# Kernel optimization log

Hardware: AMD Instinct MI355X
Metric: run time of the kernel (lower is better)

Reference implementation:

```python
import jax, jax.numpy as jnp
import numpy as np

N_NODES = 100_000
N_EDGES = 1_600_000
IN_DIM = 128
HIDDEN = 128
OUT_DIM = 64
N_LAYERS = 8
ALPHA = 0.1  # GCN2Conv alpha; beta = 1.0 since theta/layer not given


def setup_inputs() -> dict:
    key = jax.random.key(0)
    ks = jax.random.split(key, 6)
    x = jax.random.normal(ks[0], (N_NODES, IN_DIM), dtype=jnp.float32)
    edge_index = jax.random.randint(ks[1], (2, N_EDGES), 0, N_NODES, dtype=jnp.int64)
    W_in = jax.random.normal(ks[2], (IN_DIM, HIDDEN), dtype=jnp.float32) / np.sqrt(IN_DIM)
    b_in = jnp.zeros((HIDDEN,), jnp.float32)
    conv_w = jax.random.normal(ks[3], (N_LAYERS, HIDDEN, HIDDEN), dtype=jnp.float32) / np.sqrt(HIDDEN)
    W_out = jax.random.normal(ks[4], (HIDDEN, OUT_DIM), dtype=jnp.float32) / np.sqrt(HIDDEN)
    b_out = jnp.zeros((OUT_DIM,), jnp.float32)
    return {"x": x, "edge_index": edge_index, "W_in": W_in, "b_in": b_in,
            "conv_w": conv_w, "W_out": W_out, "b_out": b_out}


def reference(x, edge_index, W_in, b_in, conv_w, W_out, b_out):
    N = x.shape[0]
    # gcn_norm with self-loops: A_hat = D^-1/2 (A + I) D^-1/2
    loops = jnp.arange(N, dtype=edge_index.dtype)
    ei = jnp.concatenate([edge_index, jnp.stack([loops, loops])], axis=1)
    row, col = ei[0], ei[1]  # source, target
    deg = jax.ops.segment_sum(jnp.ones(ei.shape[1], x.dtype), col, num_segments=N)
    dinv = jnp.where(deg > 0, jax.lax.rsqrt(deg), 0.0)
    norm = dinv[row] * dinv[col]  # [E+N]

    h = jax.nn.relu(x @ W_in + b_in)  # input projection
    x0 = h  # initial residual
    for l in range(conv_w.shape[0]):
        # sparse neighbor aggregation: out[i] = sum_{(j->i)} norm * h[j]
        agg = jax.ops.segment_sum(h[row] * norm[:, None], col, num_segments=N)
        support = (1.0 - ALPHA) * agg + ALPHA * x0  # initial residual mix
        h = jax.nn.relu(support @ conv_w[l])  # beta=1 -> out = support @ W
        # dropout: identity in eval mode
    return h @ W_out + b_out
```

## Files before the change

kernel.cpp:

```cpp
#include <hip/hip_runtime.h>
#include <hip/hip_fp16.h>
#include <cstdint>
#include <cstddef>


#define HID 128
#define BKSH 9
#define RMAX 256
#define SLICE_CAP 11264

using f16x8 = __attribute__((ext_vector_type(8))) _Float16;
using f16x4 = __attribute__((ext_vector_type(4))) _Float16;
using f32x4 = __attribute__((ext_vector_type(4))) float;


__global__ __launch_bounds__(512) void k_bhist(const int* __restrict__ col, int E,
                                               int* __restrict__ bcnt, int R) {
  __shared__ int lh[RMAX];
  int tid = threadIdx.x;
  if (tid < R) lh[tid] = 0;
  __syncthreads();
  int base = blockIdx.x * 4096;
#pragma unroll
  for (int i = 0; i < 8; ++i) {
    int e = base + i * 512 + tid;
    if (e < E) atomicAdd(&lh[col[e] >> BKSH], 1);
  }
  __syncthreads();
  if (tid < R && lh[tid]) atomicAdd(&bcnt[tid], lh[tid]);
}

__global__ __launch_bounds__(256) void k_scan196(const int* __restrict__ bcnt,
                                                 int* __restrict__ gb,
                                                 int* __restrict__ gfront, int R) {
  __shared__ int s[256];
  int t = threadIdx.x;
  int v = (t < R) ? bcnt[t] : 0;
  s[t] = v;
  __syncthreads();
  for (int off = 1; off < 256; off <<= 1) {
    int a = (t >= off) ? s[t - off] : 0;
    __syncthreads();
    s[t] += a;
    __syncthreads();
  }
  int excl = s[t] - v;
  if (t < R) {
    gb[t] = excl;
    gfront[t] = excl;
  }
  if (t == 255) gb[R] = s[255];
}

__global__ __launch_bounds__(512) void k_partA(const int* __restrict__ row,
                                               const int* __restrict__ col, int E,
                                               int* __restrict__ gfront,
                                               int* __restrict__ tmp, int R) {
  __shared__ int lh[RMAX], base[RMAX], fr[RMAX];
  int tid = threadIdx.x;
  if (tid < R) { lh[tid] = 0; fr[tid] = 0; }
  __syncthreads();
  int b0 = blockIdx.x * 4096;
  int r[8], c[8], bk[8];
  bool ok[8];
#pragma unroll
  for (int i = 0; i < 8; ++i) {
    int e = b0 + i * 512 + tid;
    ok[i] = e < E;
    if (ok[i]) {
      r[i] = row[e];
      c[i] = col[e];
      bk[i] = c[i] >> BKSH;
      atomicAdd(&lh[bk[i]], 1);
    }
  }
  __syncthreads();
  if (tid < R && lh[tid] > 0) base[tid] = atomicAdd(&gfront[tid], lh[tid]);
  __syncthreads();
#pragma unroll
  for (int i = 0; i < 8; ++i) {
    if (ok[i]) {
      int o = atomicAdd(&fr[bk[i]], 1);
      tmp[base[bk[i]] + o] = (r[i] << BKSH) | (c[i] & ((1 << BKSH) - 1));
    }
  }
}

__global__ __launch_bounds__(512) void k_partB(const int* __restrict__ tmp,
                                               const int* __restrict__ gb,
                                               int* __restrict__ csr_src,
                                               int* __restrict__ row_ptr,
                                               float* __restrict__ dinv, int N, int E,
                                               int R) {
  __shared__ int h2[512], pref[512];
  __shared__ int slice[SLICE_CAP];
  int tid = threadIdx.x;
  int b = blockIdx.x;
  int lo = gb[b], hi = gb[b + 1];
  int cnt = hi - lo;
  h2[tid] = 0;
  __syncthreads();
  for (int k = tid; k < cnt; k += 512) atomicAdd(&h2[tmp[lo + k] & 511], 1);
  __syncthreads();
  int v = h2[tid];
  pref[tid] = v;
  __syncthreads();
  for (int off = 1; off < 512; off <<= 1) {
    int a = (tid >= off) ? pref[tid - off] : 0;
    __syncthreads();
    pref[tid] += a;
    __syncthreads();
  }
  int excl = pref[tid] - v;
  int node = b * 512 + tid;
  if (node < N) {
    row_ptr[node] = lo + excl;
    dinv[node] = rsqrtf((float)v + 1.0f);
  }
  if (b == R - 1 && tid == 0) row_ptr[N] = E;
  __syncthreads();
  pref[tid] = excl;
  h2[tid] = 0;
  __syncthreads();
  for (int k = tid; k < cnt; k += 512) {
    int ent = tmp[lo + k];
    int nd = ent & 511;
    int o = pref[nd] + atomicAdd(&h2[nd], 1);
    if (o < SLICE_CAP) slice[o] = ent >> BKSH;
    else csr_src[lo + o] = ent >> BKSH;
  }
  __syncthreads();
  int lim = cnt < SLICE_CAP ? cnt : SLICE_CAP;
  for (int k = tid; k < lim; k += 512) csr_src[lo + k] = slice[k];
}

__global__ void k_wprep(const float* __restrict__ Wc, const float* __restrict__ W_in,
                        const float* __restrict__ W_out, _Float16* __restrict__ Wt,
                        int L) {
  int id = blockIdx.x * blockDim.x + threadIdx.x;
  int nl = L * 16384;
  if (id < nl) {
    int l = id >> 14, r = id & 16383;
    int k = r >> 7, n = r & 127;
    Wt[(size_t)l * 16384 + n * 128 + k] = (_Float16)Wc[(size_t)l * 16384 + k * 128 + n];
  } else if (id < nl + 16384) {
    int r = id - nl;
    int k = r >> 7, n = r & 127;
    Wt[(size_t)nl + n * 128 + k] = (_Float16)W_in[k * 128 + n];
  } else if (id < nl + 16384 + 8192) {
    int r = id - nl - 16384;
    int k = r >> 6, n = r & 63;
    Wt[(size_t)(nl + 16384) + n * 128 + k] = (_Float16)W_out[k * 64 + n];
  }
}


__global__ __launch_bounds__(256) void k_aggregate(
    const _Float16* __restrict__ g, const _Float16* __restrict__ x0h,
    const float* __restrict__ dinv, const int* __restrict__ row_ptr,
    const int* __restrict__ csr_src, _Float16* __restrict__ support, int N) {
  int node = blockIdx.x * 8 + (threadIdx.x >> 5);
  if (node >= N) return;
  int lane = threadIdx.x & 31;
  int d0 = lane * 4;
  int beg = row_ptr[node], end = row_ptr[node + 1];
  float di = dinv[node];

  f16x4 v0 = *(const f16x4*)(g + (size_t)node * HID + d0);
  f16x4 xv = *(const f16x4*)(x0h + (size_t)node * HID + d0);

  float a0 = (float)v0[0], a1 = (float)v0[1];
  float a2 = (float)v0[2], a3 = (float)v0[3];

  int j = beg;
  for (; j + 8 <= end; j += 8) {
    int s0 = csr_src[j],     s1 = csr_src[j + 1], s2 = csr_src[j + 2], s3 = csr_src[j + 3];
    int s4 = csr_src[j + 4], s5 = csr_src[j + 5], s6 = csr_src[j + 6], s7 = csr_src[j + 7];
    f16x4 r0 = *(const f16x4*)(g + (size_t)s0 * HID + d0);
    f16x4 r1 = *(const f16x4*)(g + (size_t)s1 * HID + d0);
    f16x4 r2 = *(const f16x4*)(g + (size_t)s2 * HID + d0);
    f16x4 r3 = *(const f16x4*)(g + (size_t)s3 * HID + d0);
    f16x4 r4 = *(const f16x4*)(g + (size_t)s4 * HID + d0);
    f16x4 r5 = *(const f16x4*)(g + (size_t)s5 * HID + d0);
    f16x4 r6 = *(const f16x4*)(g + (size_t)s6 * HID + d0);
    f16x4 r7 = *(const f16x4*)(g + (size_t)s7 * HID + d0);
    a0 += (float)r0[0] + (float)r1[0] + (float)r2[0] + (float)r3[0] +
          (float)r4[0] + (float)r5[0] + (float)r6[0] + (float)r7[0];
    a1 += (float)r0[1] + (float)r1[1] + (float)r2[1] + (float)r3[1] +
          (float)r4[1] + (float)r5[1] + (float)r6[1] + (float)r7[1];
    a2 += (float)r0[2] + (float)r1[2] + (float)r2[2] + (float)r3[2] +
          (float)r4[2] + (float)r5[2] + (float)r6[2] + (float)r7[2];
    a3 += (float)r0[3] + (float)r1[3] + (float)r2[3] + (float)r3[3] +
          (float)r4[3] + (float)r5[3] + (float)r6[3] + (float)r7[3];
  }
  if (j + 4 <= end) {
    int s0 = csr_src[j], s1 = csr_src[j + 1], s2 = csr_src[j + 2], s3 = csr_src[j + 3];
    f16x4 r0 = *(const f16x4*)(g + (size_t)s0 * HID + d0);
    f16x4 r1 = *(const f16x4*)(g + (size_t)s1 * HID + d0);
    f16x4 r2 = *(const f16x4*)(g + (size_t)s2 * HID + d0);
    f16x4 r3 = *(const f16x4*)(g + (size_t)s3 * HID + d0);
    a0 += (float)r0[0] + (float)r1[0] + (float)r2[0] + (float)r3[0];
    a1 += (float)r0[1] + (float)r1[1] + (float)r2[1] + (float)r3[1];
    a2 += (float)r0[2] + (float)r1[2] + (float)r2[2] + (float)r3[2];
    a3 += (float)r0[3] + (float)r1[3] + (float)r2[3] + (float)r3[3];
    j += 4;
  }
  for (; j < end; ++j) {
    int s = csr_src[j];
    f16x4 r = *(const f16x4*)(g + (size_t)s * HID + d0);
    a0 += (float)r[0]; a1 += (float)r[1]; a2 += (float)r[2]; a3 += (float)r[3];
  }
  float s9 = 0.9f * di;
  f16x4 o;
  o[0] = (_Float16)(s9 * a0 + 0.1f * (float)xv[0]);
  o[1] = (_Float16)(s9 * a1 + 0.1f * (float)xv[1]);
  o[2] = (_Float16)(s9 * a2 + 0.1f * (float)xv[2]);
  o[3] = (_Float16)(s9 * a3 + 0.1f * (float)xv[3]);
  *(f16x4*)(support + (size_t)node * HID + d0) = o;
}


template <int NC, bool RELU, bool BIAS, bool AF32, bool OHALF, bool WS, bool WR>
__global__ __launch_bounds__(256) void k_mfma_gemm(const void* __restrict__ Av,
                                                   const _Float16* __restrict__ Bt,
                                                   const float* __restrict__ bias,
                                                   const float* __restrict__ dinv,
                                                   _Float16* __restrict__ Cs,
                                                   void* __restrict__ Craw, int M) {
  constexpr int NT = NC / 16;
  int tid = threadIdx.x;
  int w = tid >> 6, l = tid & 63;
  int lm = l & 15, kg = l >> 4;
  int row0 = blockIdx.x * 128 + w * 32;
  int r0 = min(row0 + lm, M - 1);
  int r1 = min(row0 + 16 + lm, M - 1);

  f32x4 acc[2][NT];
#pragma unroll
  for (int mt = 0; mt < 2; ++mt)
#pragma unroll
    for (int nt = 0; nt < NT; ++nt) acc[mt][nt] = (f32x4){0.f, 0.f, 0.f, 0.f};

#pragma unroll
  for (int ks = 0; ks < 128; ks += 32) {
    f16x8 a0, a1;
    if (AF32) {
      const float* Af = (const float*)Av;
      float4 p0 = *(const float4*)(Af + (size_t)r0 * 128 + ks + kg * 8);
      float4 p1 = *(const float4*)(Af + (size_t)r0 * 128 + ks + kg * 8 + 4);
      float4 q0 = *(const float4*)(Af + (size_t)r1 * 128 + ks + kg * 8);
      float4 q1 = *(const float4*)(Af + (size_t)r1 * 128 + ks + kg * 8 + 4);
      a0[0] = (_Float16)p0.x; a0[1] = (_Float16)p0.y; a0[2] = (_Float16)p0.z; a0[3] = (_Float16)p0.w;
      a0[4] = (_Float16)p1.x; a0[5] = (_Float16)p1.y; a0[6] = (_Float16)p1.z; a0[7] = (_Float16)p1.w;
      a1[0] = (_Float16)q0.x; a1[1] = (_Float16)q0.y; a1[2] = (_Float16)q0.z; a1[3] = (_Float16)q0.w;
      a1[4] = (_Float16)q1.x; a1[5] = (_Float16)q1.y; a1[6] = (_Float16)q1.z; a1[7] = (_Float16)q1.w;
    } else {
      const _Float16* Ah = (const _Float16*)Av;
      a0 = *(const f16x8*)(Ah + (size_t)r0 * 128 + ks + kg * 8);
      a1 = *(const f16x8*)(Ah + (size_t)r1 * 128 + ks + kg * 8);
    }
#pragma unroll
    for (int nt = 0; nt < NT; ++nt) {
      f16x8 b = *(const f16x8*)(Bt + (size_t)(nt * 16 + lm) * 128 + ks + kg * 8);
      acc[0][nt] = __builtin_amdgcn_mfma_f32_16x16x32_f16(a0, b, acc[0][nt], 0, 0, 0);
      acc[1][nt] = __builtin_amdgcn_mfma_f32_16x16x32_f16(a1, b, acc[1][nt], 0, 0, 0);
    }
  }

#pragma unroll
  for (int mt = 0; mt < 2; ++mt) {
#pragma unroll
    for (int nt = 0; nt < NT; ++nt) {
      int colc = nt * 16 + lm;
      float bv = BIAS ? bias[colc] : 0.0f;
#pragma unroll
      for (int i = 0; i < 4; ++i) {
        int r = row0 + mt * 16 + kg * 4 + i;
        if (r >= M) continue;
        float v = acc[mt][nt][i] + bv;
        if (RELU) v = fmaxf(v, 0.0f);
        if (WR) {
          if (OHALF)
            ((_Float16*)Craw)[(size_t)r * NC + colc] = (_Float16)v;
          else
            ((float*)Craw)[(size_t)r * NC + colc] = v;
        }
        if (WS) Cs[(size_t)r * NC + colc] = (_Float16)(dinv[r] * v);
      }
    }
  }
}


extern "C" void kernel_launch(void* const* d_in, const int* in_sizes, int n_in,
                              void* d_out, int out_size, void* d_ws, size_t ws_size,
                              hipStream_t stream) {
  const float* x     = (const float*)d_in[0];
  const int*   ei    = (const int*)d_in[1];
  const float* W_in  = (const float*)d_in[2];
  const float* b_in  = (const float*)d_in[3];
  const float* Wc    = (const float*)d_in[4];
  const float* W_out = (const float*)d_in[5];
  const float* b_out = (const float*)d_in[6];
  float* out = (float*)d_out;

  const int N = in_sizes[0] / HID;
  const int E = in_sizes[1] / 2;
  const int L = in_sizes[4] / (HID * HID);
  const int R = (N + 511) >> BKSH;
  const int* row = ei;
  const int* col = ei + E;

  char* p = (char*)d_ws;
  auto alloc = [&](size_t bytes) {
    char* q = p;
    p += (bytes + 255) & ~(size_t)255;
    return q;
  };
  _Float16* x0h   = (_Float16*)alloc((size_t)N * HID * 2);
  _Float16* gA    = (_Float16*)alloc((size_t)N * HID * 2);
  _Float16* gB    = (_Float16*)alloc((size_t)N * HID * 2);
  _Float16* sup16 = (_Float16*)alloc((size_t)N * HID * 2);
  _Float16* Wt    = (_Float16*)alloc((size_t)(L * 16384 + 16384 + 8192) * 2);
  int*    row_ptr = (int*)alloc((size_t)(N + 1) * 4);
  float*  dinv    = (float*)alloc((size_t)N * 4);
  int*    csr_src = (int*)alloc((size_t)E * 4);
  int*    tmp     = (int*)alloc((size_t)E * 4);
  int*    bcnt    = (int*)alloc((size_t)R * 4);
  int*    gb      = (int*)alloc((size_t)(R + 1) * 4);
  int*    gfront  = (int*)alloc((size_t)R * 4);
  (void)ws_size; (void)n_in; (void)out_size;

  const _Float16* Wt_in  = Wt + (size_t)L * 16384;
  const _Float16* Wt_out = Wt + (size_t)L * 16384 + 16384;

  hipMemsetAsync(bcnt, 0, (size_t)R * 4, stream);

  int nw = L * 16384 + 16384 + 8192;
  int nbe = (E + 4095) / 4096;
  k_wprep<<<(nw + 255) / 256, 256, 0, stream>>>(Wc, W_in, W_out, Wt, L);
  k_bhist<<<nbe, 512, 0, stream>>>(col, E, bcnt, R);
  k_scan196<<<1, 256, 0, stream>>>(bcnt, gb, gfront, R);
  k_partA<<<nbe, 512, 0, stream>>>(row, col, E, gfront, tmp, R);
  k_partB<<<R, 512, 0, stream>>>(tmp, gb, csr_src, row_ptr, dinv, N, E, R);

  int ggrid = (N + 127) / 128;
  int agrid = (N + 7) / 8;

  k_mfma_gemm<128, true, true, true, true, true, true>
      <<<ggrid, 256, 0, stream>>>(x, Wt_in, b_in, dinv, gA, x0h, N);

  _Float16* cur = gA;
  _Float16* nxt = gB;
  for (int l = 0; l < L; ++l) {
    k_aggregate<<<agrid, 256, 0, stream>>>(cur, x0h, dinv, row_ptr, csr_src, sup16, N);
    if (l < L - 1) {
      k_mfma_gemm<128, true, false, false, true, true, false>
          <<<ggrid, 256, 0, stream>>>(sup16, Wt + (size_t)l * 16384, nullptr, dinv,
                                      nxt, nullptr, N);
    } else {
      k_mfma_gemm<128, true, false, false, true, false, true>
          <<<ggrid, 256, 0, stream>>>(sup16, Wt + (size_t)l * 16384, nullptr, nullptr,
                                      nullptr, nxt, N);
    }
    _Float16* t = cur; cur = nxt; nxt = t;
  }
  k_mfma_gemm<64, false, true, false, false, false, true>
      <<<ggrid, 256, 0, stream>>>(cur, Wt_out, b_out, nullptr, nullptr, out, N);
}
```

Measured before the change: 913.6 us.

## Slice feature layout for cache-local gathers and fuse residual mix into GEMM

Stores the dinv-scaled hidden features in eight 16-column slices (slice-major), and the aggregation kernel processes one slice per block so the gathered working set per slice (100k×32B) fits in cache. The residual mix (0.9·dinv·agg + 0.1·x0) moves from the aggregation kernel into the GEMM's A-operand load. The cost targeted is random-gather traffic to HBM. In exchange, each edge list is re-read eight times and each gather is only 4 bytes per lane.

Result: slower. 1.073 ms (+17.5%).

```diff
diff --git a/kernel.cpp b/kernel.cpp
--- a/kernel.cpp
+++ b/kernel.cpp
@@ -10,7 +10,7 @@
 #define SLICE_CAP 11264
 
 using f16x8 = __attribute__((ext_vector_type(8))) _Float16;
-using f16x4 = __attribute__((ext_vector_type(4))) _Float16;
+using f16x2 = __attribute__((ext_vector_type(2))) _Float16;
 using f32x4 = __attribute__((ext_vector_type(4))) float;
 
 
@@ -156,75 +156,64 @@
 
 
 __global__ __launch_bounds__(256) void k_aggregate(
-    const _Float16* __restrict__ g, const _Float16* __restrict__ x0h,
-    const float* __restrict__ dinv, const int* __restrict__ row_ptr,
-    const int* __restrict__ csr_src, _Float16* __restrict__ support, int N) {
-  int node = blockIdx.x * 8 + (threadIdx.x >> 5);
+    const _Float16* __restrict__ g, const int* __restrict__ row_ptr,
+    const int* __restrict__ csr_src, _Float16* __restrict__ aggs, int N) {
+  int slice = blockIdx.x & 7;
+  int node = (blockIdx.x >> 3) * 32 + (threadIdx.x >> 3);
   if (node >= N) return;
-  int lane = threadIdx.x & 31;
-  int d0 = lane * 4;
+  int lane8 = threadIdx.x & 7;
+  const _Float16* gs = g + (size_t)slice * N * 16 + lane8 * 2;
   int beg = row_ptr[node], end = row_ptr[node + 1];
-  float di = dinv[node];
-
-  f16x4 v0 = *(const f16x4*)(g + (size_t)node * HID + d0);
-  f16x4 xv = *(const f16x4*)(x0h + (size_t)node * HID + d0);
-
+
+  f16x2 v0 = *(const f16x2*)(gs + (size_t)node * 16);
   float a0 = (float)v0[0], a1 = (float)v0[1];
-  float a2 = (float)v0[2], a3 = (float)v0[3];
 
   int j = beg;
   for (; j + 8 <= end; j += 8) {
     int s0 = csr_src[j],     s1 = csr_src[j + 1], s2 = csr_src[j + 2], s3 = csr_src[j + 3];
     int s4 = csr_src[j + 4], s5 = csr_src[j + 5], s6 = csr_src[j + 6], s7 = csr_src[j + 7];
-    f16x4 r0 = *(const f16x4*)(g + (size_t)s0 * HID + d0);
-    f16x4 r1 = *(const f16x4*)(g + (size_t)s1 * HID + d0);
-    f16x4 r2 = *(const f16x4*)(g + (size_t)s2 * HID + d0);
-    f16x4 r3 = *(const f16x4*)(g + (size_t)s3 * HID + d0);
-    f16x4 r4 = *(const f16x4*)(g + (size_t)s4 * HID + d0);
-    f16x4 r5 = *(const f16x4*)(g + (size_t)s5 * HID + d0);
-    f16x4 r6 = *(const f16x4*)(g + (size_t)s6 * HID + d0);
-    f16x4 r7 = *(const f16x4*)(g + (size_t)s7 * HID + d0);
+    f16x2 r0 = *(const f16x2*)(gs + (size_t)s0 * 16);
+    f16x2 r1 = *(const f16x2*)(gs + (size_t)s1 * 16);
+    f16x2 r2 = *(const f16x2*)(gs + (size_t)s2 * 16);
+    f16x2 r3 = *(const f16x2*)(gs + (size_t)s3 * 16);
+    f16x2 r4 = *(const f16x2*)(gs + (size_t)s4 * 16);
+    f16x2 r5 = *(const f16x2*)(gs + (size_t)s5 * 16);
+    f16x2 r6 = *(const f16x2*)(gs + (size_t)s6 * 16);
+    f16x2 r7 = *(const f16x2*)(gs + (size_t)s7 * 16);
     a0 += (float)r0[0] + (float)r1[0] + (float)r2[0] + (float)r3[0] +
           (float)r4[0] + (float)r5[0] + (float)r6[0] + (float)r7[0];
     a1 += (float)r0[1] + (float)r1[1] + (float)r2[1] + (float)r3[1] +
           (float)r4[1] + (float)r5[1] + (float)r6[1] + (float)r7[1];
-    a2 += (float)r0[2] + (float)r1[2] + (float)r2[2] + (float)r3[2] +
-          (float)r4[2] + (float)r5[2] + (float)r6[2] + (float)r7[2];
-    a3 += (float)r0[3] + (float)r1[3] + (float)r2[3] + (float)r3[3] +
-          (float)r4[3] + (float)r5[3] + (float)r6[3] + (float)r7[3];
   }
   if (j + 4 <= end) {
     int s0 = csr_src[j], s1 = csr_src[j + 1], s2 = csr_src[j + 2], s3 = csr_src[j + 3];
-    f16x4 r0 = *(const f16x4*)(g + (size_t)s0 * HID + d0);
-    f16x4 r1 = *(const f16x4*)(g + (size_t)s1 * HID + d0);
-    f16x4 r2 = *(const f16x4*)(g + (size_t)s2 * HID + d0);
-    f16x4 r3 = *(const f16x4*)(g + (size_t)s3 * HID + d0);
+    f16x2 r0 = *(const f16x2*)(gs + (size_t)s0 * 16);
+    f16x2 r1 = *(const f16x2*)(gs + (size_t)s1 * 16);
+    f16x2 r2 = *(const f16x2*)(gs + (size_t)s2 * 16);
+    f16x2 r3 = *(const f16x2*)(gs + (size_t)s3 * 16);
     a0 += (float)r0[0] + (float)r1[0] + (float)r2[0] + (float)r3[0];
     a1 += (float)r0[1] + (float)r1[1] + (float)r2[1] + (float)r3[1];
-    a2 += (float)r0[2] + (float)r1[2] + (float)r2[2] + (float)r3[2];
-    a3 += (float)r0[3] + (float)r1[3] + (float)r2[3] + (float)r3[3];
     j += 4;
   }
   for (; j < end; ++j) {
     int s = csr_src[j];
-    f16x4 r = *(const f16x4*)(g + (size_t)s * HID + d0);
-    a0 += (float)r[0]; a1 += (float)r[1]; a2 += (float)r[2]; a3 += (float)r[3];
-  }
-  float s9 = 0.9f * di;
-  f16x4 o;
-  o[0] = (_Float16)(s9 * a0 + 0.1f * (float)xv[0]);
-  o[1] = (_Float16)(s9 * a1 + 0.1f * (float)xv[1]);
-  o[2] = (_Float16)(s9 * a2 + 0.1f * (float)xv[2]);
-  o[3] = (_Float16)(s9 * a3 + 0.1f * (float)xv[3]);
-  *(f16x4*)(support + (size_t)node * HID + d0) = o;
-}
-
-
-template <int NC, bool RELU, bool BIAS, bool AF32, bool OHALF, bool WS, bool WR>
+    f16x2 r = *(const f16x2*)(gs + (size_t)s * 16);
+    a0 += (float)r[0];
+    a1 += (float)r[1];
+  }
+  f16x2 o;
+  o[0] = (_Float16)a0;
+  o[1] = (_Float16)a1;
+  *(f16x2*)(aggs + ((size_t)slice * N + node) * 16 + lane8 * 2) = o;
+}
+
+
+template <int NC, bool RELU, bool BIAS, bool AF32, bool OHALF, bool WS, bool WR, bool MIX>
 __global__ __launch_bounds__(256) void k_mfma_gemm(const void* __restrict__ Av,
                                                    const _Float16* __restrict__ Bt,
                                                    const float* __restrict__ bias,
                                                    const float* __restrict__ dinv,
+                                                   const _Float16* __restrict__ Xm,
                                                    _Float16* __restrict__ Cs,
                                                    void* __restrict__ Craw, int M) {
   constexpr int NT = NC / 16;
@@ -235,6 +224,12 @@
   int r0 = min(row0 + lm, M - 1);
   int r1 = min(row0 + 16 + lm, M - 1);
 
+  float dv0 = 0.0f, dv1 = 0.0f;
+  if (MIX) {
+    dv0 = 0.9f * dinv[r0];
+    dv1 = 0.9f * dinv[r1];
+  }
+
   f32x4 acc[2][NT];
 #pragma unroll
   for (int mt = 0; mt < 2; ++mt)
@@ -244,7 +239,20 @@
 #pragma unroll
   for (int ks = 0; ks < 128; ks += 32) {
     f16x8 a0, a1;
-    if (AF32) {
+    if (MIX) {
+      int k0 = ks + kg * 8;
+      int sl = k0 >> 4, off = k0 & 15;
+      const _Float16* Ag = (const _Float16*)Av;
+      f16x8 c0 = *(const f16x8*)(Ag + ((size_t)sl * M + r0) * 16 + off);
+      f16x8 c1 = *(const f16x8*)(Ag + ((size_t)sl * M + r1) * 16 + off);
+      f16x8 x0v = *(const f16x8*)(Xm + (size_t)r0 * 128 + k0);
+      f16x8 x1v = *(const f16x8*)(Xm + (size_t)r1 * 128 + k0);
+#pragma unroll
+      for (int i = 0; i < 8; ++i) {
+        a0[i] = (_Float16)(dv0 * (float)c0[i] + 0.1f * (float)x0v[i]);
+        a1[i] = (_Float16)(dv1 * (float)c1[i] + 0.1f * (float)x1v[i]);
+      }
+    } else if (AF32) {
       const float* Af = (const float*)Av;
       float4 p0 = *(const float4*)(Af + (size_t)r0 * 128 + ks + kg * 8);
       float4 p1 = *(const float4*)(Af + (size_t)r0 * 128 + ks + kg * 8 + 4);
@@ -285,7 +293,7 @@
           else
             ((float*)Craw)[(size_t)r * NC + colc] = v;
         }
-        if (WS) Cs[(size_t)r * NC + colc] = (_Float16)(dinv[r] * v);
+        if (WS) Cs[((size_t)nt * M + r) * 16 + lm] = (_Float16)(dinv[r] * v);
       }
     }
   }
@@ -320,7 +328,8 @@
   _Float16* x0h   = (_Float16*)alloc((size_t)N * HID * 2);
   _Float16* gA    = (_Float16*)alloc((size_t)N * HID * 2);
   _Float16* gB    = (_Float16*)alloc((size_t)N * HID * 2);
-  _Float16* sup16 = (_Float16*)alloc((size_t)N * HID * 2);
+  _Float16* aggs  = (_Float16*)alloc((size_t)N * HID * 2);
+  _Float16* h16   = (_Float16*)alloc((size_t)N * HID * 2);
   _Float16* Wt    = (_Float16*)alloc((size_t)(L * 16384 + 16384 + 8192) * 2);
   int*    row_ptr = (int*)alloc((size_t)(N + 1) * 4);
   float*  dinv    = (float*)alloc((size_t)N * 4);
@@ -345,26 +354,27 @@
   k_partB<<<R, 512, 0, stream>>>(tmp, gb, csr_src, row_ptr, dinv, N, E, R);
 
   int ggrid = (N + 127) / 128;
-  int agrid = (N + 7) / 8;
-
-  k_mfma_gemm<128, true, true, true, true, true, true>
-      <<<ggrid, 256, 0, stream>>>(x, Wt_in, b_in, dinv, gA, x0h, N);
+  int agrid = ((N + 31) / 32) * 8;
+
+  k_mfma_gemm<128, true, true, true, true, true, true, false>
+      <<<ggrid, 256, 0, stream>>>(x, Wt_in, b_in, dinv, nullptr, gA, x0h, N);
 
   _Float16* cur = gA;
   _Float16* nxt = gB;
   for (int l = 0; l < L; ++l) {
-    k_aggregate<<<agrid, 256, 0, stream>>>(cur, x0h, dinv, row_ptr, csr_src, sup16, N);
+    k_aggregate<<<agrid, 256, 0, stream>>>(cur, row_ptr, csr_src, aggs, N);
     if (l < L - 1) {
-      k_mfma_gemm<128, true, false, false, true, true, false>
-          <<<ggrid, 256, 0, stream>>>(sup16, Wt + (size_t)l * 16384, nullptr, dinv,
-                                      nxt, nullptr, N);
+      k_mfma_gemm<128, true, false, false, true, true, false, true>
+          <<<ggrid, 256, 0, stream>>>(aggs, Wt + (size_t)l * 16384, nullptr, dinv,
+                                      x0h, nxt, nullptr, N);
+      _Float16* t = cur; cur = nxt; nxt = t;
     } else {
-      k_mfma_gemm<128, true, false, false, true, false, true>
-          <<<ggrid, 256, 0, stream>>>(sup16, Wt + (size_t)l * 16384, nullptr, nullptr,
-                                      nullptr, nxt, N);
-    }
-    _Float16* t = cur; cur = nxt; nxt = t;
-  }
-  k_mfma_gemm<64, false, true, false, false, false, true>
-      <<<ggrid, 256, 0, stream>>>(cur, Wt_out, b_out, nullptr, nullptr, out, N);
-}
+      k_mfma_gemm<128, true, false, false, true, false, true, true>
+          <<<ggrid, 256, 0, stream>>>(aggs, Wt + (size_t)l * 16384, nullptr, dinv,
+                                      x0h, nullptr, h16, N);
+    }
+  }
+  k_mfma_gemm<64, false, true, false, false, false, true, false>
+      <<<ggrid, 256, 0, stream>>>(h16, Wt_out, b_out, nullptr, nullptr, nullptr,
+                                  out, N);
+}
```
